# Optimization experiments

Hardware: AMD Instinct MI355X
Metric: run time of the kernel (lower is better)

Reference implementation:

```python
import jax, jax.numpy as jnp
import numpy as np

P_FACTOR = 3.0   # config['p_factor']
EPS = 1e-12      # torch F.normalize eps

def _l2_normalize(x):
    return x / jnp.maximum(jnp.linalg.norm(x, axis=-1, keepdims=True), EPS)

def _l1_normalize(x):
    return x / jnp.maximum(jnp.sum(jnp.abs(x), axis=-1, keepdims=True), EPS)

def setup_inputs() -> dict:
    key = jax.random.key(0)
    k = jax.random.split(key, 6)
    B, N_EX, D_IN, D_FEAT, N_LAB, D_CLS = 4096, 16384, 1024, 256, 28, 64
    features = jax.random.normal(k[0], (B, D_IN), jnp.float32)
    labels = jax.random.uniform(k[1], (B, N_LAB), jnp.float32)            # BCE targets in [0,1]
    ex_features = jax.random.normal(k[2], (N_EX, D_IN), jnp.float32)
    ex_classes = jax.random.uniform(k[3], (N_EX, N_LAB), jnp.float32)     # class memberships
    g_w = jax.random.normal(k[4], (D_FEAT, D_IN), jnp.float32) * 0.02     # Linear(in=1024,out=256,bias=False)
    class_reps = jax.random.uniform(k[5], (N_LAB, D_CLS), jnp.float32) * 2.0 - 1.0  # rand*2-1
    return {"features": features, "labels": labels, "ex_features": ex_features,
            "ex_classes": ex_classes, "g_w": g_w, "class_reps": class_reps}

def reference(features, labels, ex_features, ex_classes, g_w, class_reps):
    # g projection (use_g=True, no bias)
    f = features @ g_w.T          # [B, D_FEAT]
    ef = ex_features @ g_w.T      # [N_EX, D_FEAT]
    # exemplar class representations: L1-normalized memberships @ class_reps
    ex_class_reps = _l1_normalize(ex_classes) @ class_reps   # [N_EX, D_CLS]
    # cosine similarity between queries and exemplars
    s = _l2_normalize(f) @ _l2_normalize(ef).T               # [B, N_EX]
    # power-sign activation then L1 normalize over exemplars
    a = _l1_normalize(jnp.sign(s) * jnp.abs(s) ** P_FACTOR)  # [B, N_EX]
    # weighted exemplar aggregation
    echo = a @ ex_class_reps                                  # [B, D_CLS]
    # negative euclidean distances to class representations (cdist)
    diff = echo[:, None, :] - class_reps[None, :, :]          # [B, N_LAB, D_CLS]
    neg_dists = -jnp.sqrt(jnp.sum(diff * diff, axis=-1))      # [B, N_LAB]
    # BCEWithLogitsLoss (mean reduction)
    loss = jnp.mean(-(labels * jax.nn.log_sigmoid(neg_dists)
                      + (1.0 - labels) * jax.nn.log_sigmoid(-neg_dists)))
    return (loss, neg_dists)
```

## Files before the change

kernel.cpp:

```cpp
#include <hip/hip_runtime.h>


typedef __bf16 bf16x8 __attribute__((ext_vector_type(8)));
typedef __bf16 bf16x4 __attribute__((ext_vector_type(4)));
typedef float  f32x4  __attribute__((ext_vector_type(4)));

__device__ __forceinline__ f32x4 f4zero() { f32x4 z = {0.f, 0.f, 0.f, 0.f}; return z; }

__device__ __forceinline__ f32x4 mfma16(bf16x8 a, bf16x8 b, f32x4 c) {
  return __builtin_amdgcn_mfma_f32_16x16x32_bf16(a, b, c, 0, 0, 0);
}

__device__ __forceinline__ bf16x8 load8f(const float* p) {
  f32x4 a = *(const f32x4*)p;
  f32x4 b = *(const f32x4*)(p + 4);
  bf16x8 r;
  r[0] = (__bf16)a[0]; r[1] = (__bf16)a[1]; r[2] = (__bf16)a[2]; r[3] = (__bf16)a[3];
  r[4] = (__bf16)b[0]; r[5] = (__bf16)b[1]; r[6] = (__bf16)b[2]; r[7] = (__bf16)b[3];
  return r;
}

__device__ __forceinline__ void async16(const void* g, void* l) {
  __builtin_amdgcn_global_load_lds(
      (const __attribute__((address_space(1))) unsigned int*)g,
      (__attribute__((address_space(3))) unsigned int*)l, 16, 0, 0);
}

__global__ void zero_f32(float* __restrict__ p, int n) {
  for (int i = blockIdx.x * 256 + threadIdx.x; i < n; i += gridDim.x * 256) p[i] = 0.f;
}

__global__ void fill_sentinel(float* __restrict__ out, int n) {
  for (int i = blockIdx.x * 256 + threadIdx.x; i < n; i += gridDim.x * 256) out[i] = -1.0f;
}

__global__ void convert_w(const float* __restrict__ W, __bf16* __restrict__ W2) {
  int i = blockIdx.x * 256 + threadIdx.x;
  int ks  = i >> 11;
  int idx = i & 2047;
  int row = idx >> 3;
  int c4  = (idx & 7) ^ (row & 7);
  *(bf16x8*)(W2 + (size_t)i * 8) = load8f(W + (size_t)row * 1024 + ks * 64 + c4 * 8);
}

__global__ __launch_bounds__(256, 3)
void proj_l2norm(const float* __restrict__ Xa, const float* __restrict__ Xb,
                 const __bf16* __restrict__ W2,
                 __bf16* __restrict__ Pa, __bf16* __restrict__ Pb) {
  __shared__ __align__(16) __bf16 Xs[32 * 72];
  __shared__ __align__(16) __bf16 Ws[256 * 64];
  __shared__ float nrmW[4 * 32];
  __shared__ float invn[32];

  const int tid = threadIdx.x;
  const int w = tid >> 6, lane = tid & 63;
  const int quad = lane >> 4, l15 = lane & 15;
  const int sw = l15 & 7;

  const float* X;
  __bf16* P;
  int row0;
  if (blockIdx.x < 512) { X = Xa; P = Pa; row0 = blockIdx.x * 32; }
  else                  { X = Xb; P = Pb; row0 = (blockIdx.x - 512) * 32; }

  f32x4 acc[2][4];
#pragma unroll
  for (int i = 0; i < 2; i++)
#pragma unroll
    for (int j = 0; j < 4; j++) acc[i][j] = f4zero();

  for (int ks = 0; ks < 16; ks++) {
    __syncthreads();
    {
      int row = tid >> 3, c8 = tid & 7;
      *(bf16x8*)(Xs + row * 72 + c8 * 8) =
          load8f(X + (size_t)(row0 + row) * 1024 + ks * 64 + c8 * 8);
    }
    {
      const __bf16* w2k = W2 + (size_t)ks * 16384;
#pragma unroll
      for (int rep = 0; rep < 8; rep++) {
        int idx = rep * 256 + tid;
        async16(w2k + idx * 8, Ws + idx * 8);
      }
    }
    __syncthreads();
#pragma unroll
    for (int ksub = 0; ksub < 2; ksub++) {
      bf16x8 af[2], bfr[4];
#pragma unroll
      for (int mb = 0; mb < 2; mb++)
        af[mb] = *(bf16x8*)(Xs + (mb * 16 + l15) * 72 + ksub * 32 + quad * 8);
#pragma unroll
      for (int nb = 0; nb < 4; nb++) {
        int c4 = ksub * 4 + quad;
        bfr[nb] = *(bf16x8*)(Ws + (w * 64 + nb * 16 + l15) * 64 + (c4 ^ sw) * 8);
      }
#pragma unroll
      for (int mb = 0; mb < 2; mb++)
#pragma unroll
        for (int nb = 0; nb < 4; nb++)
          acc[mb][nb] = mfma16(af[mb], bfr[nb], acc[mb][nb]);
    }
  }

  float part[2][4];
#pragma unroll
  for (int mb = 0; mb < 2; mb++)
#pragma unroll
    for (int r = 0; r < 4; r++) {
      float s = 0.f;
#pragma unroll
      for (int nb = 0; nb < 4; nb++) { float v = acc[mb][nb][r]; s += v * v; }
      part[mb][r] = s;
    }
#pragma unroll
  for (int m = 1; m < 16; m <<= 1)
#pragma unroll
    for (int mb = 0; mb < 2; mb++)
#pragma unroll
      for (int r = 0; r < 4; r++) part[mb][r] += __shfl_xor(part[mb][r], m, 64);

  if (l15 == 0) {
#pragma unroll
    for (int mb = 0; mb < 2; mb++)
#pragma unroll
      for (int r = 0; r < 4; r++)
        nrmW[w * 32 + mb * 16 + quad * 4 + r] = part[mb][r];
  }
  __syncthreads();
  if (tid < 32) {
    float s = nrmW[tid] + nrmW[32 + tid] + nrmW[64 + tid] + nrmW[96 + tid];
    invn[tid] = 1.0f / fmaxf(sqrtf(s), 1e-12f);
  }
  __syncthreads();
#pragma unroll
  for (int mb = 0; mb < 2; mb++)
#pragma unroll
    for (int nb = 0; nb < 4; nb++)
#pragma unroll
      for (int r = 0; r < 4; r++) {
        int row = mb * 16 + quad * 4 + r;
        int col = w * 64 + nb * 16 + l15;
        P[(size_t)(row0 + row) * 256 + col] = (__bf16)(acc[mb][nb][r] * invn[row]);
      }
}

__global__ void build_vt(const float* __restrict__ exc, __bf16* __restrict__ vT) {
  int e = blockIdx.x * 256 + threadIdx.x;
  float m[28];
  float s = 0.f;
#pragma unroll
  for (int j = 0; j < 28; j++) {
    m[j] = exc[(size_t)e * 28 + j];
    s += fabsf(m[j]);
  }
  float inv = 1.0f / fmaxf(s, 1e-12f);
#pragma unroll
  for (int j = 0; j < 28; j++) vT[(size_t)j * 16384 + e] = (__bf16)(m[j] * inv);
#pragma unroll
  for (int j = 28; j < 32; j++) vT[(size_t)j * 16384 + e] = (__bf16)0.0f;
}

__global__ __launch_bounds__(256, 2)
void fused_sim(const __bf16* __restrict__ fn, const __bf16* __restrict__ efn,
               const __bf16* __restrict__ vTg,
               float* __restrict__ tT, float* __restrict__ r_acc) {
  __shared__ __align__(16) __bf16 Ks[64 * 256];
  __shared__ __align__(16) __bf16 Vs[32 * 72];
  __shared__ __align__(16) __bf16 Us[128 * 72];

  const int tid = threadIdx.x, w = tid >> 6, lane = tid & 63;
  const int quad = lane >> 4, l15 = lane & 15;
  const int wy = w >> 1, wx = w & 1;
  const int swk = l15 & 7;
  const int chunk = blockIdx.x & 15, mtile = blockIdx.x >> 4;
  const int q0 = mtile * 128;
  const int e_base = chunk * 1024;

  int koff[8];
#pragma unroll
  for (int rep = 0; rep < 8; rep++) {
    int idx = rep * 256 + tid;
    int row = idx >> 5;
    int c5  = (idx & 31) ^ (row & 7);
    koff[rep] = row * 256 + c5 * 8;
  }

  bf16x8 qf[8][4];
#pragma unroll
  for (int ks = 0; ks < 8; ks++)
#pragma unroll
    for (int nb = 0; nb < 4; nb++)
      qf[ks][nb] = *(const bf16x8*)(fn + (size_t)(q0 + wx * 64 + nb * 16 + l15) * 256 +
                                    ks * 32 + quad * 8);

  float r_part[4] = {0.f, 0.f, 0.f, 0.f};
  f32x4 accp[2][2];
#pragma unroll
  for (int a = 0; a < 2; a++)
#pragma unroll
    for (int b = 0; b < 2; b++) accp[a][b] = f4zero();

  for (int t = 0; t < 16; t++) {
    const int e_t = e_base + t * 64;

    __syncthreads();
    {
      const __bf16* src = efn + (size_t)e_t * 256;
#pragma unroll
      for (int rep = 0; rep < 8; rep++)
        async16(src + koff[rep], Ks + (rep * 256 + tid) * 8);
    }
    {
      int row = tid >> 3, c8 = tid & 7;
      *(bf16x8*)(Vs + row * 72 + c8 * 8) =
          *(const bf16x8*)(vTg + (size_t)row * 16384 + e_t + c8 * 8);
    }
    __syncthreads();

    f32x4 accs[2][4];
#pragma unroll
    for (int a = 0; a < 2; a++)
#pragma unroll
      for (int b = 0; b < 4; b++) accs[a][b] = f4zero();
#pragma unroll
    for (int ks = 0; ks < 8; ks++) {
      bf16x8 af[2];
#pragma unroll
      for (int mb = 0; mb < 2; mb++)
        af[mb] = *(bf16x8*)(Ks + (wy * 32 + mb * 16 + l15) * 256 +
                            ((ks * 4 + quad) ^ swk) * 8);
#pragma unroll
      for (int mb = 0; mb < 2; mb++)
#pragma unroll
        for (int nb = 0; nb < 4; nb++)
          accs[mb][nb] = mfma16(af[mb], qf[ks][nb], accs[mb][nb]);
    }

#pragma unroll
    for (int mb = 0; mb < 2; mb++) {
      const int eo = wy * 32 + mb * 16 + quad * 4;
#pragma unroll
      for (int nb = 0; nb < 4; nb++) {
        const int q = wx * 64 + nb * 16 + l15;
        bf16x4 pk;
#pragma unroll
        for (int r = 0; r < 4; r++) {
          float s = accs[mb][nb][r];
          __bf16 ub = (__bf16)(s * s * s);
          pk[r] = ub;
          r_part[nb] += fabsf((float)ub);
        }
        *(bf16x4*)(Us + q * 72 + eo) = pk;
      }
    }
    __syncthreads();

#pragma unroll
    for (int ks = 0; ks < 2; ks++) {
      bf16x8 vf[2], uf[2];
#pragma unroll
      for (int cb = 0; cb < 2; cb++)
        vf[cb] = *(bf16x8*)(Vs + (cb * 16 + l15) * 72 + ks * 32 + quad * 8);
#pragma unroll
      for (int qb = 0; qb < 2; qb++)
        uf[qb] = *(bf16x8*)(Us + (w * 32 + qb * 16 + l15) * 72 + ks * 32 + quad * 8);
#pragma unroll
      for (int cb = 0; cb < 2; cb++)
#pragma unroll
        for (int qb = 0; qb < 2; qb++)
          accp[cb][qb] = mfma16(vf[cb], uf[qb], accp[cb][qb]);
    }
  }

#pragma unroll
  for (int nb = 0; nb < 4; nb++) {
    float v = r_part[nb];
    v += __shfl_xor(v, 16, 64);
    v += __shfl_xor(v, 32, 64);
    if (quad == 0) atomicAdd(&r_acc[q0 + wx * 64 + nb * 16 + l15], v);
  }
#pragma unroll
  for (int cb = 0; cb < 2; cb++)
#pragma unroll
    for (int qb = 0; qb < 2; qb++)
#pragma unroll
      for (int r = 0; r < 4; r++)
        atomicAdd(&tT[(size_t)(cb * 16 + quad * 4 + r) * 4096 + q0 + w * 32 + qb * 16 + l15],
                  accp[cb][qb][r]);
}

__global__ __launch_bounds__(256, 4)
void finalize(const float* __restrict__ tT, const float* __restrict__ r_acc,
              const float* __restrict__ creps, const float* __restrict__ labels,
              float* __restrict__ loss_acc, float* __restrict__ out) {
  __shared__ __align__(16) float cr[28 * 64];
  __shared__ float wsum[4];
  const int tid = threadIdx.x, w = tid >> 6, lane = tid & 63;
  for (int i = tid; i < 28 * 64; i += 256) cr[i] = creps[i];
  __syncthreads();

  const int q = blockIdx.x * 4 + w;
  float tval = 0.f;
  if (lane < 28) tval = tT[(size_t)lane * 4096 + q];
  tval *= 1.0f / fmaxf(r_acc[q], 1e-12f);

  float echo = 0.f;
#pragma unroll
  for (int j = 0; j < 28; j++)
    echo = fmaf(__shfl(tval, j, 64), cr[j * 64 + lane], echo);

  float dj = 0.f;
#pragma unroll
  for (int j = 0; j < 28; j++) {
    float df = echo - cr[j * 64 + lane];
    float d2 = df * df;
#pragma unroll
    for (int m = 1; m < 64; m <<= 1) d2 += __shfl_xor(d2, m, 64);
    if (lane == j) dj = sqrtf(d2);
  }

  float lsum = 0.f;
  if (lane < 28) {
    out[1 + (size_t)q * 28 + lane] = -dj;
    float y = labels[(size_t)q * 28 + lane];
    lsum = fmaf(y, dj, log1pf(expf(-dj)));
  }
#pragma unroll
  for (int m = 1; m < 64; m <<= 1) lsum += __shfl_xor(lsum, m, 64);
  if (lane == 0) wsum[w] = lsum;
  __syncthreads();
  if (tid == 0) atomicAdd(loss_acc, wsum[0] + wsum[1] + wsum[2] + wsum[3]);
}

__global__ void write_loss(const float* __restrict__ loss_acc, float* __restrict__ out) {
  out[0] = loss_acc[0] * (1.0f / 114688.0f);
}

extern "C" void kernel_launch(void* const* d_in, const int* in_sizes, int n_in,
                              void* d_out, int out_size, void* d_ws, size_t ws_size,
                              hipStream_t stream) {
  const float* features = nullptr;
  const float* labels   = nullptr;
  const float* ex_feat  = nullptr;
  const float* ex_cls   = nullptr;
  const float* g_w      = nullptr;
  const float* creps    = nullptr;
  for (int i = 0; i < n_in; i++) {
    switch (in_sizes[i]) {
      case 4194304:  features = (const float*)d_in[i]; break;
      case 114688:   labels   = (const float*)d_in[i]; break;
      case 16777216: ex_feat  = (const float*)d_in[i]; break;
      case 458752:   ex_cls   = (const float*)d_in[i]; break;
      case 262144:   g_w      = (const float*)d_in[i]; break;
      case 1792:     creps    = (const float*)d_in[i]; break;
      default: break;
    }
  }
  float* out = (float*)d_out;

  if (!features || !labels || !ex_feat || !ex_cls || !g_w || !creps ||
      ws_size < (16ull << 20)) {
    fill_sentinel<<<256, 256, 0, stream>>>(out, out_size);
    return;
  }

  char* ws = (char*)d_ws;
  __bf16* f_n   = (__bf16*)(ws);
  __bf16* ef_n  = (__bf16*)(ws + (2ull << 20));
  __bf16* vT    = (__bf16*)(ws + (10ull << 20));
  float*  tT    = (float*) (ws + (11ull << 20));
  float*  r_acc = tT + 32 * 4096;
  float*  lossp = r_acc + 4096;
  __bf16* W2    = (__bf16*)(ws + (12ull << 20));

  zero_f32<<<528, 256, 0, stream>>>(tT, 32 * 4096 + 4096 + 1);
  convert_w<<<128, 256, 0, stream>>>(g_w, W2);

  proj_l2norm<<<640, 256, 0, stream>>>(ex_feat, features, W2, ef_n, f_n);
  build_vt<<<64, 256, 0, stream>>>(ex_cls, vT);
  fused_sim<<<512, 256, 0, stream>>>(f_n, ef_n, vT, tT, r_acc);
  finalize<<<1024, 256, 0, stream>>>(tT, r_acc, creps, labels, lossp, out);
  write_loss<<<1, 1, 0, stream>>>(lossp, out);
}
```

Measured before the change: 224.3 us.

## Double-buffer projection and similarity loads, merge prep kernels into one launch

Merges the three small setup kernels (zeroing, weight conversion, vT build) into a single prep launch to cut launch overhead. proj_l2norm now double-buffers its X and W tiles so the next k-slice loads while MFMAs run, at the cost of twice the LDS and a lower occupancy bound (3 to 2). fused_sim prefetches the next exemplar K tile and V tile asynchronously, overlapping them with the cube/aggregation phase. It also replaces __syncthreads with explicit waitcnt+barrier variants and swizzles the V tile layout. The K buffer stays single and is reloaded after a barrier, which relies on the new barrier placement being correct.

```diff
diff --git a/kernel.cpp b/kernel.cpp
--- a/kernel.cpp
+++ b/kernel.cpp
@@ -26,29 +26,55 @@
       (__attribute__((address_space(3))) unsigned int*)l, 16, 0, 0);
 }
 
-__global__ void zero_f32(float* __restrict__ p, int n) {
-  for (int i = blockIdx.x * 256 + threadIdx.x; i < n; i += gridDim.x * 256) p[i] = 0.f;
+__device__ __forceinline__ void bar_lgkm() {
+  asm volatile("s_waitcnt lgkmcnt(0)" ::: "memory");
+  __builtin_amdgcn_s_barrier();
+}
+__device__ __forceinline__ void bar_all() {
+  asm volatile("s_waitcnt vmcnt(0) lgkmcnt(0)" ::: "memory");
+  __builtin_amdgcn_s_barrier();
 }
 
 __global__ void fill_sentinel(float* __restrict__ out, int n) {
   for (int i = blockIdx.x * 256 + threadIdx.x; i < n; i += gridDim.x * 256) out[i] = -1.0f;
 }
 
-__global__ void convert_w(const float* __restrict__ W, __bf16* __restrict__ W2) {
-  int i = blockIdx.x * 256 + threadIdx.x;
-  int ks  = i >> 11;
-  int idx = i & 2047;
-  int row = idx >> 3;
-  int c4  = (idx & 7) ^ (row & 7);
-  *(bf16x8*)(W2 + (size_t)i * 8) = load8f(W + (size_t)row * 1024 + ks * 64 + c4 * 8);
-}
-
-__global__ __launch_bounds__(256, 3)
+__global__ void prep(const float* __restrict__ exc, __bf16* __restrict__ vT,
+                     const float* __restrict__ W, __bf16* __restrict__ W2,
+                     float* __restrict__ zp, int zn) {
+  const int b = blockIdx.x, tid = threadIdx.x;
+  if (b < 64) {
+    int e = b * 256 + tid;
+    float m[28];
+    float s = 0.f;
+#pragma unroll
+    for (int j = 0; j < 28; j++) {
+      m[j] = exc[(size_t)e * 28 + j];
+      s += fabsf(m[j]);
+    }
+    float inv = 1.0f / fmaxf(s, 1e-12f);
+#pragma unroll
+    for (int j = 0; j < 28; j++) vT[(size_t)j * 16384 + e] = (__bf16)(m[j] * inv);
+#pragma unroll
+    for (int j = 28; j < 32; j++) vT[(size_t)j * 16384 + e] = (__bf16)0.0f;
+  } else if (b < 192) {
+    int i = (b - 64) * 256 + tid;
+    int ks  = i >> 11;
+    int idx = i & 2047;
+    int row = idx >> 3;
+    int c4  = (idx & 7) ^ (row & 7);
+    *(bf16x8*)(W2 + (size_t)i * 8) = load8f(W + (size_t)row * 1024 + ks * 64 + c4 * 8);
+  } else {
+    for (int i = (b - 192) * 256 + tid; i < zn; i += (gridDim.x - 192) * 256) zp[i] = 0.f;
+  }
+}
+
+__global__ __launch_bounds__(256, 2)
 void proj_l2norm(const float* __restrict__ Xa, const float* __restrict__ Xb,
                  const __bf16* __restrict__ W2,
                  __bf16* __restrict__ Pa, __bf16* __restrict__ Pb) {
-  __shared__ __align__(16) __bf16 Xs[32 * 72];
-  __shared__ __align__(16) __bf16 Ws[256 * 64];
+  __shared__ __align__(16) __bf16 Xs[2][32 * 72];
+  __shared__ __align__(16) __bf16 Ws[2][256 * 64];
   __shared__ float nrmW[4 * 32];
   __shared__ float invn[32];
 
@@ -56,6 +82,7 @@
   const int w = tid >> 6, lane = tid & 63;
   const int quad = lane >> 4, l15 = lane & 15;
   const int sw = l15 & 7;
+  const int xrow = tid >> 3, xc8 = tid & 7;
 
   const float* X;
   __bf16* P;
@@ -63,38 +90,48 @@
   if (blockIdx.x < 512) { X = Xa; P = Pa; row0 = blockIdx.x * 32; }
   else                  { X = Xb; P = Pb; row0 = (blockIdx.x - 512) * 32; }
 
+  const float* xsrc = X + (size_t)(row0 + xrow) * 1024 + xc8 * 8;
+
+  *(bf16x8*)(&Xs[0][xrow * 72 + xc8 * 8]) = load8f(xsrc);
+#pragma unroll
+  for (int rep = 0; rep < 8; rep++) {
+    int idx = rep * 256 + tid;
+    async16(W2 + idx * 8, &Ws[0][idx * 8]);
+  }
+
   f32x4 acc[2][4];
 #pragma unroll
   for (int i = 0; i < 2; i++)
 #pragma unroll
     for (int j = 0; j < 4; j++) acc[i][j] = f4zero();
 
+  bar_all();
+
+  int cur = 0;
   for (int ks = 0; ks < 16; ks++) {
-    __syncthreads();
-    {
-      int row = tid >> 3, c8 = tid & 7;
-      *(bf16x8*)(Xs + row * 72 + c8 * 8) =
-          load8f(X + (size_t)(row0 + row) * 1024 + ks * 64 + c8 * 8);
-    }
-    {
-      const __bf16* w2k = W2 + (size_t)ks * 16384;
+    const int nxt = cur ^ 1;
+    f32x4 xa, xb;
+    if (ks < 15) {
+      const float* xp = xsrc + (ks + 1) * 64;
+      xa = *(const f32x4*)xp;
+      xb = *(const f32x4*)(xp + 4);
+      const __bf16* w2k = W2 + (size_t)(ks + 1) * 16384;
 #pragma unroll
       for (int rep = 0; rep < 8; rep++) {
         int idx = rep * 256 + tid;
-        async16(w2k + idx * 8, Ws + idx * 8);
+        async16(w2k + idx * 8, &Ws[nxt][idx * 8]);
       }
     }
-    __syncthreads();
 #pragma unroll
     for (int ksub = 0; ksub < 2; ksub++) {
       bf16x8 af[2], bfr[4];
 #pragma unroll
       for (int mb = 0; mb < 2; mb++)
-        af[mb] = *(bf16x8*)(Xs + (mb * 16 + l15) * 72 + ksub * 32 + quad * 8);
+        af[mb] = *(bf16x8*)(&Xs[cur][(mb * 16 + l15) * 72 + ksub * 32 + quad * 8]);
 #pragma unroll
       for (int nb = 0; nb < 4; nb++) {
         int c4 = ksub * 4 + quad;
-        bfr[nb] = *(bf16x8*)(Ws + (w * 64 + nb * 16 + l15) * 64 + (c4 ^ sw) * 8);
+        bfr[nb] = *(bf16x8*)(&Ws[cur][(w * 64 + nb * 16 + l15) * 64 + (c4 ^ sw) * 8]);
       }
 #pragma unroll
       for (int mb = 0; mb < 2; mb++)
@@ -102,6 +139,14 @@
         for (int nb = 0; nb < 4; nb++)
           acc[mb][nb] = mfma16(af[mb], bfr[nb], acc[mb][nb]);
     }
+    if (ks < 15) {
+      bf16x8 r;
+      r[0] = (__bf16)xa[0]; r[1] = (__bf16)xa[1]; r[2] = (__bf16)xa[2]; r[3] = (__bf16)xa[3];
+      r[4] = (__bf16)xb[0]; r[5] = (__bf16)xb[1]; r[6] = (__bf16)xb[2]; r[7] = (__bf16)xb[3];
+      *(bf16x8*)(&Xs[nxt][xrow * 72 + xc8 * 8]) = r;
+    }
+    bar_all();
+    cur = nxt;
   }
 
   float part[2][4];
@@ -146,28 +191,12 @@
       }
 }
 
-__global__ void build_vt(const float* __restrict__ exc, __bf16* __restrict__ vT) {
-  int e = blockIdx.x * 256 + threadIdx.x;
-  float m[28];
-  float s = 0.f;
-#pragma unroll
-  for (int j = 0; j < 28; j++) {
-    m[j] = exc[(size_t)e * 28 + j];
-    s += fabsf(m[j]);
-  }
-  float inv = 1.0f / fmaxf(s, 1e-12f);
-#pragma unroll
-  for (int j = 0; j < 28; j++) vT[(size_t)j * 16384 + e] = (__bf16)(m[j] * inv);
-#pragma unroll
-  for (int j = 28; j < 32; j++) vT[(size_t)j * 16384 + e] = (__bf16)0.0f;
-}
-
 __global__ __launch_bounds__(256, 2)
 void fused_sim(const __bf16* __restrict__ fn, const __bf16* __restrict__ efn,
                const __bf16* __restrict__ vTg,
                float* __restrict__ tT, float* __restrict__ r_acc) {
   __shared__ __align__(16) __bf16 Ks[64 * 256];
-  __shared__ __align__(16) __bf16 Vs[32 * 72];
+  __shared__ __align__(16) __bf16 Vs[2][32 * 64];
   __shared__ __align__(16) __bf16 Us[128 * 72];
 
   const int tid = threadIdx.x, w = tid >> 6, lane = tid & 63;
@@ -186,6 +215,16 @@
     int c5  = (idx & 31) ^ (row & 7);
     koff[rep] = row * 256 + c5 * 8;
   }
+  const int vrow = tid >> 3;
+  const int vcs  = (tid & 7) ^ (vrow & 7);
+  const size_t vsrc0 = (size_t)vrow * 16384 + e_base + vcs * 8;
+
+  {
+    const __bf16* src = efn + (size_t)e_base * 256;
+#pragma unroll
+    for (int rep = 0; rep < 8; rep++) async16(src + koff[rep], Ks + (rep * 256 + tid) * 8);
+    async16(vTg + vsrc0, &Vs[0][tid * 8]);
+  }
 
   bf16x8 qf[8][4];
 #pragma unroll
@@ -202,23 +241,10 @@
 #pragma unroll
     for (int b = 0; b < 2; b++) accp[a][b] = f4zero();
 
+  bar_all();
+
+  int cur = 0;
   for (int t = 0; t < 16; t++) {
-    const int e_t = e_base + t * 64;
-
-    __syncthreads();
-    {
-      const __bf16* src = efn + (size_t)e_t * 256;
-#pragma unroll
-      for (int rep = 0; rep < 8; rep++)
-        async16(src + koff[rep], Ks + (rep * 256 + tid) * 8);
-    }
-    {
-      int row = tid >> 3, c8 = tid & 7;
-      *(bf16x8*)(Vs + row * 72 + c8 * 8) =
-          *(const bf16x8*)(vTg + (size_t)row * 16384 + e_t + c8 * 8);
-    }
-    __syncthreads();
-
     f32x4 accs[2][4];
 #pragma unroll
     for (int a = 0; a < 2; a++)
@@ -236,6 +262,16 @@
 #pragma unroll
         for (int nb = 0; nb < 4; nb++)
           accs[mb][nb] = mfma16(af[mb], qf[ks][nb], accs[mb][nb]);
+    }
+
+    bar_lgkm();
+
+    if (t < 15) {
+      const __bf16* src = efn + (size_t)(e_base + (t + 1) * 64) * 256;
+#pragma unroll
+      for (int rep = 0; rep < 8; rep++)
+        async16(src + koff[rep], Ks + (rep * 256 + tid) * 8);
+      async16(vTg + vsrc0 + (t + 1) * 64, &Vs[cur ^ 1][tid * 8]);
     }
 
 #pragma unroll
@@ -255,14 +291,15 @@
         *(bf16x4*)(Us + q * 72 + eo) = pk;
       }
     }
-    __syncthreads();
+
+    bar_lgkm();
 
 #pragma unroll
     for (int ks = 0; ks < 2; ks++) {
       bf16x8 vf[2], uf[2];
 #pragma unroll
       for (int cb = 0; cb < 2; cb++)
-        vf[cb] = *(bf16x8*)(Vs + (cb * 16 + l15) * 72 + ks * 32 + quad * 8);
+        vf[cb] = *(bf16x8*)(&Vs[cur][(cb * 16 + l15) * 64 + ((ks * 4 + quad) ^ swk) * 8]);
 #pragma unroll
       for (int qb = 0; qb < 2; qb++)
         uf[qb] = *(bf16x8*)(Us + (w * 32 + qb * 16 + l15) * 72 + ks * 32 + quad * 8);
@@ -272,6 +309,9 @@
         for (int qb = 0; qb < 2; qb++)
           accp[cb][qb] = mfma16(vf[cb], uf[qb], accp[cb][qb]);
     }
+
+    bar_all();
+    cur ^= 1;
   }
 
 #pragma unroll
@@ -375,11 +415,9 @@
   float*  lossp = r_acc + 4096;
   __bf16* W2    = (__bf16*)(ws + (12ull << 20));
 
-  zero_f32<<<528, 256, 0, stream>>>(tT, 32 * 4096 + 4096 + 1);
-  convert_w<<<128, 256, 0, stream>>>(g_w, W2);
+  prep<<<720, 256, 0, stream>>>(ex_cls, vT, g_w, W2, tT, 32 * 4096 + 4096 + 1);
 
   proj_l2norm<<<640, 256, 0, stream>>>(ex_feat, features, W2, ef_n, f_n);
-  build_vt<<<64, 256, 0, stream>>>(ex_cls, vT);
   fused_sim<<<512, 256, 0, stream>>>(f_n, ef_n, vT, tT, r_acc);
   finalize<<<1024, 256, 0, stream>>>(tT, r_acc, creps, labels, lossp, out);
   write_loss<<<1, 1, 0, stream>>>(lossp, out);
```

New measurement: 227.7 us. No clear change (+1.5%).
